# Kernel optimization log

Hardware: AMD Instinct MI355X
Metric: run time of the kernel (lower is better)

Reference implementation:

```python
import jax, jax.numpy as jnp
import numpy as np

KV_POOL = 2


def setup_inputs() -> dict:
    key = jax.random.key(0)
    ks = jax.random.split(key, 12)
    B, C1, C2, H, W, D = 8, 256, 512, 64, 64, 64
    s = 0.02
    return {
        "x1": jax.random.normal(ks[0], (B, C1, H, W), jnp.float32),
        "x2": jax.random.normal(ks[1], (B, C2, H, W), jnp.float32),
        "Wq": jax.random.normal(ks[2], (D, C1), jnp.float32) * s,
        "bq": jnp.zeros((D,), jnp.float32),
        "Wk": jax.random.normal(ks[3], (D, C2), jnp.float32) * s,
        "bk": jnp.zeros((D,), jnp.float32),
        "Wv": jax.random.normal(ks[4], (D, C2), jnp.float32) * s,
        "bv": jnp.zeros((D,), jnp.float32),
        "Wo": jax.random.normal(ks[5], (C1, D), jnp.float32) * s,
        "bo": jnp.zeros((C1,), jnp.float32),
    }


def reference(x1, x2, Wq, bq, Wk, bk, Wv, bv, Wo, bo):
    B, C1, H, W = x1.shape
    D = Wq.shape[0]
    # adaptive_avg_pool2d to (H//2, W//2) with even dims == 2x2 mean pool
    Bs, C2, H2, W2 = x2.shape
    x2p = x2.reshape(Bs, C2, H2 // KV_POOL, KV_POOL, W2 // KV_POOL, KV_POOL).mean(axis=(3, 5))
    # 1x1 convs as channel matmuls; flatten spatial dims
    Q = jnp.einsum('bchw,dc->bhwd', x1, Wq).reshape(B, H * W, D) + bq          # [B,N,D]
    K = jnp.einsum('bchw,dc->bhwd', x2p, Wk).reshape(B, -1, D) + bk            # [B,M,D]
    V = jnp.einsum('bchw,dc->bhwd', x2p, Wv).reshape(B, -1, D) + bv            # [B,M,D]
    attn = jax.nn.softmax(jnp.einsum('bnd,bmd->bnm', Q, K), axis=-1)           # [B,N,M]
    out = jnp.einsum('bnm,bmd->bnd', attn, V)                                  # [B,N,D]
    y = jnp.einsum('bnd,cd->bnc', out, Wo) + bo                                # [B,N,C1]
    y = y.reshape(B, H, W, C1).transpose(0, 3, 1, 2)                           # [B,C1,H,W]
    return x1 + y
```

## Files before the change

### kernel.cpp

```cpp
#include <hip/hip_runtime.h>
#include <hip/hip_bf16.h>

typedef __bf16 bf16x4 __attribute__((ext_vector_type(4)));
typedef __bf16 bf16x8 __attribute__((ext_vector_type(8)));
typedef float f32x16 __attribute__((ext_vector_type(16)));
typedef unsigned int u32x4 __attribute__((ext_vector_type(4)));

static constexpr int Bc = 8, C1 = 256, C2 = 512, Hh = 64, Ww = 64, Dd = 64;
static constexpr int Nn = 4096, Mm = 1024;

#define MFMA __builtin_amdgcn_mfma_f32_32x32x16_bf16

__device__ __forceinline__ uint32_t pkbf(float a, float b) {
  union { __bf16 h[2]; uint32_t u; } x;
  x.h[0] = (__bf16)a; x.h[1] = (__bf16)b;
  return x.u;
}

__device__ __forceinline__ void pack16(const float* p, bf16x8& f0, bf16x8& f1) {
  uint32_t w01 = pkbf(p[0], p[1]),   w23 = pkbf(p[2], p[3]);
  uint32_t w45 = pkbf(p[4], p[5]),   w67 = pkbf(p[6], p[7]);
  uint32_t w89 = pkbf(p[8], p[9]),   wab = pkbf(p[10], p[11]);
  uint32_t wcd = pkbf(p[12], p[13]), wef = pkbf(p[14], p[15]);
  auto s0 = __builtin_amdgcn_permlane32_swap(w01, w45, false, false);
  auto s1 = __builtin_amdgcn_permlane32_swap(w23, w67, false, false);
  auto s2 = __builtin_amdgcn_permlane32_swap(w89, wcd, false, false);
  auto s3 = __builtin_amdgcn_permlane32_swap(wab, wef, false, false);
  u32x4 q0 = {s0[0], s1[0], s0[1], s1[1]};
  u32x4 q1 = {s2[0], s3[0], s2[1], s3[1]};
  f0 = __builtin_bit_cast(bf16x8, q0);
  f1 = __builtin_bit_cast(bf16x8, q1);
}


__global__ __launch_bounds__(256) void k_prep_w(
    const float* __restrict__ Wq, const float* __restrict__ Wk,
    const float* __restrict__ Wv, const float* __restrict__ Wo,
    __bf16* __restrict__ wqb, __bf16* __restrict__ wkb,
    __bf16* __restrict__ wvb, __bf16* __restrict__ wob) {
  int i = blockIdx.x * 256 + threadIdx.x;
  if (i < 16384) wqb[i] = (__bf16)Wq[i];
  else if (i < 49152) wkb[i - 16384] = (__bf16)Wk[i - 16384];
  else if (i < 81920) wvb[i - 49152] = (__bf16)Wv[i - 49152];
  else if (i < 98304) wob[i - 81920] = (__bf16)Wo[i - 81920];
}

__global__ __launch_bounds__(256) void k_qproj(
    const float* __restrict__ x1, const __bf16* __restrict__ wqb,
    const float* __restrict__ bq, __bf16* __restrict__ qfb) {
  __shared__ __align__(16) __bf16 lds[64 * 264];
  const int b = blockIdx.y, n0 = blockIdx.x * 64, tid = threadIdx.x;
#pragma unroll 4
  for (int it = 0; it < 64; ++it) {
    int c = it * 4 + (tid >> 6);
    int j = tid & 63;
    lds[j * 264 + c] = (__bf16)x1[(size_t)(b * C1 + c) * Nn + n0 + j];
  }
  __syncthreads();
  const int w = tid >> 6, l = tid & 63, h = l >> 5, nl = l & 31;
  const int nsub = w & 1, dh = w >> 1;
  const __bf16* arow = lds + (nsub * 32 + nl) * 264;
  const __bf16* wrow = wqb + (dh * 32 + nl) * C1 + 8 * h;
  f32x16 acc = {};
#pragma unroll
  for (int ks = 0; ks < 16; ++ks) {
    bf16x8 a = *(const bf16x8*)(arow + ks * 16 + 8 * h);
    bf16x8 bb = *(const bf16x8*)(wrow + ks * 16);
    acc = MFMA(a, bb, acc, 0, 0, 0);
  }
  const int d = dh * 32 + nl;
  const float bias = bq[d];
  __bf16* qdst = qfb + (size_t)b * Nn * Dd + (size_t)((n0 >> 5) + nsub) * 2048 +
                 (d >> 4) * 512 + ((d >> 3) & 1) * 256 + (d & 7);
#pragma unroll
  for (int r = 0; r < 16; ++r) {
    int mrow = (r & 3) + 8 * (r >> 2) + 4 * h;
    qdst[mrow * 8] = (__bf16)(acc[r] + bias);
  }
}

__global__ __launch_bounds__(256) void k_kvproj(
    const float* __restrict__ x2, const __bf16* __restrict__ wkb,
    const __bf16* __restrict__ wvb, const float* __restrict__ bk,
    const float* __restrict__ bv, __bf16* __restrict__ kfb,
    __bf16* __restrict__ vfb) {
  __shared__ __align__(16) __bf16 lds[32 * 520];
  __shared__ __align__(16) __bf16 vlds[64 * 40];
  const int b = blockIdx.y, h2 = blockIdx.x, tid = threadIdx.x;
#pragma unroll 4
  for (int it = 0; it < 64; ++it) {
    int c = it * 8 + (tid >> 5);
    int j = tid & 31;
    const float* p = x2 + ((size_t)(b * C2 + c) * Hh + 2 * h2) * Ww + 2 * j;
    float2 v0 = *(const float2*)p;
    float2 v1 = *(const float2*)(p + Ww);
    lds[j * 520 + c] = (__bf16)((v0.x + v0.y + v1.x + v1.y) * 0.25f);
  }
  __syncthreads();
  const int w = tid >> 6, l = tid & 63, h = l >> 5, nl = l & 31;
  const int isv = w >> 1, dh = w & 1;
  const __bf16* arow = lds + nl * 520;
  const __bf16* wrow = (isv ? wvb : wkb) + (dh * 32 + nl) * C2 + 8 * h;
  f32x16 acc = {};
#pragma unroll
  for (int ks = 0; ks < 32; ++ks) {
    bf16x8 a = *(const bf16x8*)(arow + ks * 16 + 8 * h);
    bf16x8 bb = *(const bf16x8*)(wrow + ks * 16);
    acc = MFMA(a, bb, acc, 0, 0, 0);
  }
  const int d = dh * 32 + nl;
  const float bias = isv ? bv[d] : bk[d];
  if (!isv) {
    __bf16* kdst = kfb + (size_t)b * Mm * Dd + (size_t)h2 * 2048 +
                   (d >> 4) * 512 + ((d >> 3) & 1) * 256 + (d & 7);
#pragma unroll
    for (int r = 0; r < 16; ++r) {
      int mr = (r & 3) + 8 * (r >> 2) + 4 * h;
      kdst[mr * 8] = (__bf16)(acc[r] + bias);
    }
  } else {
#pragma unroll
    for (int r = 0; r < 16; ++r) {
      int mr = (r & 3) + 8 * (r >> 2) + 4 * h;
      vlds[d * 40 + mr] = (__bf16)(acc[r] + bias);
    }
  }
  __syncthreads();
  const int dd = tid >> 2, q = tid & 3;
  bf16x8 vv = *(const bf16x8*)(vlds + dd * 40 + q * 8);
  const int c = (q >> 1) * 2 + (dd >> 5);
  const int ll = (q & 1) * 32 + (dd & 31);
  *(bf16x8*)(vfb + (size_t)b * Mm * Dd + (size_t)h2 * 2048 + c * 512 + ll * 8) = vv;
}

template <int S>
__global__ __launch_bounds__(256) void k_attn_part(
    const __bf16* __restrict__ qfb, const __bf16* __restrict__ kfb,
    const __bf16* __restrict__ vfb, __bf16* __restrict__ po,
    float* __restrict__ pml) {
  __shared__ __align__(16) __bf16 kls[2][2048];
  __shared__ __align__(16) __bf16 vls[2][2048];
  const int lin = blockIdx.x;
  const int b = lin & 7, rest = lin >> 3, nblk = rest & 31, sp = rest >> 5;
  const int tid = threadIdx.x;
  const int w = tid >> 6, l = tid & 63, h = l >> 5, nl = l & 31;
  const int n = nblk * 128 + w * 32 + nl;
  constexpr int NT = Mm / S / 32;
  const int t0 = sp * NT;

  const __bf16* qt = qfb + (size_t)b * Nn * Dd + (size_t)(nblk * 4 + w) * 2048 + l * 8;
  bf16x8 qf0 = *(const bf16x8*)(qt);
  bf16x8 qf1 = *(const bf16x8*)(qt + 512);
  bf16x8 qf2 = *(const bf16x8*)(qt + 1024);
  bf16x8 qf3 = *(const bf16x8*)(qt + 1536);

  const __bf16* kgb = kfb + (size_t)b * Mm * Dd + (size_t)t0 * 2048 + w * 512 + l * 8;
  const __bf16* vgb = vfb + (size_t)b * Mm * Dd + (size_t)t0 * 2048 + w * 512 + l * 8;

  bf16x8 kcur = *(const bf16x8*)kgb;
  bf16x8 vcur = *(const bf16x8*)vgb;

  f32x16 o0 = {}, o1 = {};
  float lsum = 0.f;
  const int wofs = w * 512 + l * 8;

#pragma unroll
  for (int i = 0; i < NT; ++i) {
    const int cur = i & 1;
    *(bf16x8*)(&kls[cur][wofs]) = kcur;
    *(bf16x8*)(&vls[cur][wofs]) = vcur;
    __syncthreads();
    if (i + 1 < NT) {
      kcur = *(const bf16x8*)(kgb + (size_t)(i + 1) * 2048);
      vcur = *(const bf16x8*)(vgb + (size_t)(i + 1) * 2048);
    }
    bf16x8 ka0 = *(const bf16x8*)(&kls[cur][l * 8]);
    bf16x8 ka1 = *(const bf16x8*)(&kls[cur][512 + l * 8]);
    bf16x8 ka2 = *(const bf16x8*)(&kls[cur][1024 + l * 8]);
    bf16x8 ka3 = *(const bf16x8*)(&kls[cur][1536 + l * 8]);
    bf16x8 v00 = *(const bf16x8*)(&vls[cur][l * 8]);
    bf16x8 v10 = *(const bf16x8*)(&vls[cur][512 + l * 8]);
    bf16x8 v01 = *(const bf16x8*)(&vls[cur][1024 + l * 8]);
    bf16x8 v11 = *(const bf16x8*)(&vls[cur][1536 + l * 8]);
    f32x16 s = {};
    s = MFMA(ka0, qf0, s, 0, 0, 0);
    s = MFMA(ka1, qf1, s, 0, 0, 0);
    s = MFMA(ka2, qf2, s, 0, 0, 0);
    s = MFMA(ka3, qf3, s, 0, 0, 0);
    float p[16];
#pragma unroll
    for (int r = 0; r < 16; ++r) p[r] = __expf(s[r]);
    float u0 = (p[0] + p[1]) + (p[2] + p[3]);
    float u1 = (p[4] + p[5]) + (p[6] + p[7]);
    float u2 = (p[8] + p[9]) + (p[10] + p[11]);
    float u3 = (p[12] + p[13]) + (p[14] + p[15]);
    lsum += (u0 + u1) + (u2 + u3);
    bf16x8 pb0, pb1;
    pack16(p, pb0, pb1);
    o0 = MFMA(v00, pb0, o0, 0, 0, 0);
    o1 = MFMA(v10, pb0, o1, 0, 0, 0);
    o0 = MFMA(v01, pb1, o0, 0, 0, 0);
    o1 = MFMA(v11, pb1, o1, 0, 0, 0);
    __syncthreads();
  }

  const float ltot = lsum + __shfl_xor(lsum, 32);
  __bf16* ob = po + (size_t)(b * S + sp) * 16 * Nn * 4 + (size_t)n * 4;
#pragma unroll
  for (int q = 0; q < 4; ++q) {
    bf16x4 t0v, t1v;
#pragma unroll
    for (int e = 0; e < 4; ++e) {
      t0v[e] = (__bf16)o0[q * 4 + e];
      t1v[e] = (__bf16)o1[q * 4 + e];
    }
    *(bf16x4*)(ob + (size_t)(2 * q + h) * Nn * 4) = t0v;
    *(bf16x4*)(ob + (size_t)(8 + 2 * q + h) * Nn * 4) = t1v;
  }
  if (h == 0) pml[(size_t)(b * S + sp) * Nn + n] = ltot;
}

template <int S>
__global__ __launch_bounds__(256) void k_attn_comb(
    const float* __restrict__ x1, const __bf16* __restrict__ po,
    const float* __restrict__ pml, const __bf16* __restrict__ wob,
    const float* __restrict__ bo, float* __restrict__ out) {
  const int lin = blockIdx.x;
  const int b = lin & 7, rest = lin >> 3, nblk = rest & 31, ctg = rest >> 5;
  const int tid = threadIdx.x;
  const int w = tid >> 6, l = tid & 63, h = l >> 5, nl = l & 31;
  const int n = nblk * 128 + w * 32 + nl;

  float L = 0.f;
#pragma unroll
  for (int s = 0; s < S; ++s)
    L += pml[(size_t)(b * S + s) * Nn + n];
  const float inv = 1.f / L;

  float o[32];
#pragma unroll
  for (int r = 0; r < 32; ++r) o[r] = 0.f;
#pragma unroll
  for (int s = 0; s < S; ++s) {
    const __bf16* ob = po + (size_t)(b * S + s) * 16 * Nn * 4 + (size_t)n * 4;
#pragma unroll
    for (int q = 0; q < 4; ++q) {
      bf16x4 v0 = *(const bf16x4*)(ob + (size_t)(2 * q + h) * Nn * 4);
      bf16x4 v1 = *(const bf16x4*)(ob + (size_t)(8 + 2 * q + h) * Nn * 4);
#pragma unroll
      for (int e = 0; e < 4; ++e) {
        o[q * 4 + e] += (float)v0[e];
        o[16 + q * 4 + e] += (float)v1[e];
      }
    }
  }

  bf16x8 obf[4];
#pragma unroll
  for (int a2 = 0; a2 < 2; ++a2) {
    float ov[16];
#pragma unroll
    for (int r = 0; r < 16; ++r) ov[r] = o[a2 * 16 + r] * inv;
    pack16(ov, obf[a2 * 2], obf[a2 * 2 + 1]);
  }

  const float* x1r = x1 + (size_t)b * C1 * Nn + n;
  float* outr = out + (size_t)b * C1 * Nn + n;
  const __bf16* wobase = wob + (size_t)nl * Dd + 8 * h;
#pragma unroll
  for (int ci = 0; ci < 4; ++ci) {
    const int ct = ctg * 4 + ci;
    f32x16 y = {};
    const __bf16* wr = wobase + (size_t)ct * 32 * Dd;
#pragma unroll
    for (int ks = 0; ks < 4; ++ks) {
      bf16x8 a = *(const bf16x8*)(wr + ks * 16);
      y = MFMA(a, obf[ks], y, 0, 0, 0);
    }
#pragma unroll
    for (int r = 0; r < 16; ++r) {
      int c = ct * 32 + (r & 3) + 8 * (r >> 2) + 4 * h;
      size_t idx = (size_t)c * Nn;
      outr[idx] = y[r] + bo[c] + x1r[idx];
    }
  }
}

__global__ __launch_bounds__(256) void k_attn(
    const float* __restrict__ x1, const __bf16* __restrict__ qfb,
    const __bf16* __restrict__ kfb, const __bf16* __restrict__ vfb,
    const __bf16* __restrict__ wob, const float* __restrict__ bo,
    float* __restrict__ out) {
  const int b = blockIdx.y, tid = threadIdx.x;
  const int w = tid >> 6, l = tid & 63, h = l >> 5, nl = l & 31;
  const int n = blockIdx.x * 128 + w * 32 + nl;

  const __bf16* qt = qfb + (size_t)b * Nn * Dd + (size_t)(blockIdx.x * 4 + w) * 2048 + l * 8;
  bf16x8 qf0 = *(const bf16x8*)(qt);
  bf16x8 qf1 = *(const bf16x8*)(qt + 512);
  bf16x8 qf2 = *(const bf16x8*)(qt + 1024);
  bf16x8 qf3 = *(const bf16x8*)(qt + 1536);

  f32x16 o0 = {}, o1 = {};
  float mrun = -INFINITY, lsum = 0.f;

  const __bf16* kb_ = kfb + (size_t)b * Mm * Dd + l * 8;
  const __bf16* vb_ = vfb + (size_t)b * Mm * Dd + l * 8;

  for (int t = 0; t < 32; ++t) {
    const __bf16* kt = kb_ + (size_t)t * 2048;
    const __bf16* vt = vb_ + (size_t)t * 2048;
    bf16x8 ka0 = *(const bf16x8*)(kt);
    bf16x8 ka1 = *(const bf16x8*)(kt + 512);
    bf16x8 ka2 = *(const bf16x8*)(kt + 1024);
    bf16x8 ka3 = *(const bf16x8*)(kt + 1536);
    bf16x8 v00 = *(const bf16x8*)(vt);
    bf16x8 v10 = *(const bf16x8*)(vt + 512);
    bf16x8 v01 = *(const bf16x8*)(vt + 1024);
    bf16x8 v11 = *(const bf16x8*)(vt + 1536);
    f32x16 s = {};
    s = MFMA(ka0, qf0, s, 0, 0, 0);
    s = MFMA(ka1, qf1, s, 0, 0, 0);
    s = MFMA(ka2, qf2, s, 0, 0, 0);
    s = MFMA(ka3, qf3, s, 0, 0, 0);
    float tmax = s[0];
#pragma unroll
    for (int r = 1; r < 16; ++r) tmax = fmaxf(tmax, s[r]);
    tmax = fmaxf(tmax, __shfl_xor(tmax, 32));
    const float mnew = fmaxf(mrun, tmax);
    const float scale = __expf(mrun - mnew);
    float p[16], psum = 0.f;
#pragma unroll
    for (int r = 0; r < 16; ++r) { p[r] = __expf(s[r] - mnew); psum += p[r]; }
    lsum = lsum * scale + psum;
    mrun = mnew;
#pragma unroll
    for (int r = 0; r < 16; ++r) { o0[r] *= scale; o1[r] *= scale; }
    bf16x8 pb0, pb1;
    pack16(p, pb0, pb1);
    o0 = MFMA(v00, pb0, o0, 0, 0, 0);
    o1 = MFMA(v10, pb0, o1, 0, 0, 0);
    o0 = MFMA(v01, pb1, o0, 0, 0, 0);
    o1 = MFMA(v11, pb1, o1, 0, 0, 0);
  }

  const float ltot = lsum + __shfl_xor(lsum, 32);
  const float inv = 1.f / ltot;

  bf16x8 ob[4];
#pragma unroll
  for (int a2 = 0; a2 < 2; ++a2) {
    float ov[16];
#pragma unroll
    for (int r = 0; r < 16; ++r) ov[r] = (a2 ? o1[r] : o0[r]) * inv;
    pack16(ov, ob[a2 * 2], ob[a2 * 2 + 1]);
  }

  const float* x1r = x1 + (size_t)b * C1 * Nn + n;
  float* outr = out + (size_t)b * C1 * Nn + n;
  const __bf16* wobase = wob + (size_t)nl * Dd + 8 * h;
#pragma unroll 2
  for (int ct = 0; ct < 8; ++ct) {
    f32x16 y = {};
    const __bf16* wr = wobase + (size_t)ct * 32 * Dd;
#pragma unroll
    for (int ks = 0; ks < 4; ++ks) {
      bf16x8 a = *(const bf16x8*)(wr + ks * 16);
      y = MFMA(a, ob[ks], y, 0, 0, 0);
    }
#pragma unroll
    for (int r = 0; r < 16; ++r) {
      int c = ct * 32 + (r & 3) + 8 * (r >> 2) + 4 * h;
      size_t idx = (size_t)c * Nn;
      outr[idx] = y[r] + bo[c] + x1r[idx];
    }
  }
}

extern "C" void kernel_launch(void* const* d_in, const int* in_sizes, int n_in,
                              void* d_out, int out_size, void* d_ws,
                              size_t ws_size, hipStream_t stream) {
  const float* x1 = (const float*)d_in[0];
  const float* x2 = (const float*)d_in[1];
  const float* Wq = (const float*)d_in[2];
  const float* bq = (const float*)d_in[3];
  const float* Wk = (const float*)d_in[4];
  const float* bk = (const float*)d_in[5];
  const float* Wv = (const float*)d_in[6];
  const float* bv = (const float*)d_in[7];
  const float* Wo = (const float*)d_in[8];
  const float* bo = (const float*)d_in[9];
  float* out = (float*)d_out;
  char* ws = (char*)d_ws;

  __bf16* wqb = (__bf16*)(ws);
  __bf16* wkb = (__bf16*)(ws + 32768);
  __bf16* wvb = (__bf16*)(ws + 98304);
  __bf16* wob = (__bf16*)(ws + 163840);
  __bf16* qfb = (__bf16*)(ws + 196608);
  __bf16* kfb = (__bf16*)(ws + 4390912);
  __bf16* vfb = (__bf16*)(ws + 5439488);
  __bf16* po  = (__bf16*)(ws + 6488064);
  const size_t ws8 = 6488064ull + 33554432ull + 1048576ull;
  const size_t ws4 = 6488064ull + 16777216ull + 524288ull;

  hipLaunchKernelGGL(k_prep_w, dim3(384), dim3(256), 0, stream,
                     Wq, Wk, Wv, Wo, wqb, wkb, wvb, wob);
  hipLaunchKernelGGL(k_qproj, dim3(64, 8), dim3(256), 0, stream,
                     x1, wqb, bq, qfb);
  hipLaunchKernelGGL(k_kvproj, dim3(32, 8), dim3(256), 0, stream,
                     x2, wkb, wvb, bk, bv, kfb, vfb);
  if (ws_size >= ws8) {
    float* pml = (float*)(ws + 6488064 + 33554432);
    hipLaunchKernelGGL(k_attn_part<8>, dim3(32 * 8 * 8), dim3(256), 0, stream,
                       qfb, kfb, vfb, po, pml);
    hipLaunchKernelGGL(k_attn_comb<8>, dim3(32 * 8 * 2), dim3(256), 0, stream,
                       x1, po, pml, wob, bo, out);
  } else if (ws_size >= ws4) {
    float* pml = (float*)(ws + 6488064 + 16777216);
    hipLaunchKernelGGL(k_attn_part<4>, dim3(32 * 8 * 4), dim3(256), 0, stream,
                       qfb, kfb, vfb, po, pml);
    hipLaunchKernelGGL(k_attn_comb<4>, dim3(32 * 8 * 2), dim3(256), 0, stream,
                       x1, po, pml, wob, bo, out);
  } else {
    hipLaunchKernelGGL(k_attn, dim3(32, 8), dim3(256), 0, stream,
                       x1, qfb, kfb, vfb, wob, bo, out);
  }
}
```

Baseline: 67.63 us.

## Fuse projections into one kernel, convert weights inline, drop LDS staging in attention

Removes the separate weight-conversion kernel by converting fp32 weights to bf16 on the fly at load time. Merges the Q and K/V projection kernels into a single launch that splits work by block index. In the partial attention kernel, each wave now loads the full K/V tile directly from global memory into registers with prefetching, replacing the shared-memory staging and its two barriers per step. This cuts launch count and synchronisation, but every wave now re-reads K/V from global memory or cache and weight conversion is repeated per block.

```diff
diff --git a/kernel.cpp b/kernel.cpp
--- a/kernel.cpp
+++ b/kernel.cpp
@@ -15,6 +15,15 @@
   union { __bf16 h[2]; uint32_t u; } x;
   x.h[0] = (__bf16)a; x.h[1] = (__bf16)b;
   return x.u;
+}
+
+__device__ __forceinline__ bf16x8 cvt8(const float* __restrict__ p) {
+  float4 a = *(const float4*)p;
+  float4 b2 = *(const float4*)(p + 4);
+  bf16x8 r;
+  r[0] = (__bf16)a.x; r[1] = (__bf16)a.y; r[2] = (__bf16)a.z; r[3] = (__bf16)a.w;
+  r[4] = (__bf16)b2.x; r[5] = (__bf16)b2.y; r[6] = (__bf16)b2.z; r[7] = (__bf16)b2.w;
+  return r;
 }
 
 __device__ __forceinline__ void pack16(const float* p, bf16x8& f0, bf16x8& f1) {
@@ -33,104 +42,93 @@
 }
 
 
-__global__ __launch_bounds__(256) void k_prep_w(
-    const float* __restrict__ Wq, const float* __restrict__ Wk,
-    const float* __restrict__ Wv, const float* __restrict__ Wo,
-    __bf16* __restrict__ wqb, __bf16* __restrict__ wkb,
-    __bf16* __restrict__ wvb, __bf16* __restrict__ wob) {
-  int i = blockIdx.x * 256 + threadIdx.x;
-  if (i < 16384) wqb[i] = (__bf16)Wq[i];
-  else if (i < 49152) wkb[i - 16384] = (__bf16)Wk[i - 16384];
-  else if (i < 81920) wvb[i - 49152] = (__bf16)Wv[i - 49152];
-  else if (i < 98304) wob[i - 81920] = (__bf16)Wo[i - 81920];
-}
-
-__global__ __launch_bounds__(256) void k_qproj(
-    const float* __restrict__ x1, const __bf16* __restrict__ wqb,
-    const float* __restrict__ bq, __bf16* __restrict__ qfb) {
-  __shared__ __align__(16) __bf16 lds[64 * 264];
-  const int b = blockIdx.y, n0 = blockIdx.x * 64, tid = threadIdx.x;
+__global__ __launch_bounds__(256) void k_proj(
+    const float* __restrict__ x1, const float* __restrict__ x2,
+    const float* __restrict__ Wq, const float* __restrict__ bq,
+    const float* __restrict__ Wk, const float* __restrict__ bk,
+    const float* __restrict__ Wv, const float* __restrict__ bv,
+    __bf16* __restrict__ qfb, __bf16* __restrict__ kfb,
+    __bf16* __restrict__ vfb) {
+  __shared__ __align__(16) __bf16 lds[32 * 520 + 64 * 40];
+  const int bx = blockIdx.x, b = blockIdx.y, tid = threadIdx.x;
+  const int w = tid >> 6, l = tid & 63, h = l >> 5, nl = l & 31;
+
+  if (bx < 64) {
+    const int n0 = bx * 64;
 #pragma unroll 4
-  for (int it = 0; it < 64; ++it) {
-    int c = it * 4 + (tid >> 6);
-    int j = tid & 63;
-    lds[j * 264 + c] = (__bf16)x1[(size_t)(b * C1 + c) * Nn + n0 + j];
-  }
-  __syncthreads();
-  const int w = tid >> 6, l = tid & 63, h = l >> 5, nl = l & 31;
-  const int nsub = w & 1, dh = w >> 1;
-  const __bf16* arow = lds + (nsub * 32 + nl) * 264;
-  const __bf16* wrow = wqb + (dh * 32 + nl) * C1 + 8 * h;
-  f32x16 acc = {};
-#pragma unroll
-  for (int ks = 0; ks < 16; ++ks) {
-    bf16x8 a = *(const bf16x8*)(arow + ks * 16 + 8 * h);
-    bf16x8 bb = *(const bf16x8*)(wrow + ks * 16);
-    acc = MFMA(a, bb, acc, 0, 0, 0);
-  }
-  const int d = dh * 32 + nl;
-  const float bias = bq[d];
-  __bf16* qdst = qfb + (size_t)b * Nn * Dd + (size_t)((n0 >> 5) + nsub) * 2048 +
-                 (d >> 4) * 512 + ((d >> 3) & 1) * 256 + (d & 7);
-#pragma unroll
-  for (int r = 0; r < 16; ++r) {
-    int mrow = (r & 3) + 8 * (r >> 2) + 4 * h;
-    qdst[mrow * 8] = (__bf16)(acc[r] + bias);
-  }
-}
-
-__global__ __launch_bounds__(256) void k_kvproj(
-    const float* __restrict__ x2, const __bf16* __restrict__ wkb,
-    const __bf16* __restrict__ wvb, const float* __restrict__ bk,
-    const float* __restrict__ bv, __bf16* __restrict__ kfb,
-    __bf16* __restrict__ vfb) {
-  __shared__ __align__(16) __bf16 lds[32 * 520];
-  __shared__ __align__(16) __bf16 vlds[64 * 40];
-  const int b = blockIdx.y, h2 = blockIdx.x, tid = threadIdx.x;
+    for (int it = 0; it < 64; ++it) {
+      int c = it * 4 + (tid >> 6);
+      int j = tid & 63;
+      lds[j * 264 + c] = (__bf16)x1[(size_t)(b * C1 + c) * Nn + n0 + j];
+    }
+    __syncthreads();
+    const int nsub = w & 1, dh = w >> 1;
+    const __bf16* arow = lds + (nsub * 32 + nl) * 264;
+    const float* wrow = Wq + (size_t)(dh * 32 + nl) * C1 + 8 * h;
+    f32x16 acc = {};
+#pragma unroll
+    for (int ks = 0; ks < 16; ++ks) {
+      bf16x8 a = *(const bf16x8*)(arow + ks * 16 + 8 * h);
+      bf16x8 bb = cvt8(wrow + ks * 16);
+      acc = MFMA(a, bb, acc, 0, 0, 0);
+    }
+    const int d = dh * 32 + nl;
+    const float bias = bq[d];
+    __bf16* qdst = qfb + (size_t)b * Nn * Dd + (size_t)((n0 >> 5) + nsub) * 2048 +
+                   (d >> 4) * 512 + ((d >> 3) & 1) * 256 + (d & 7);
+#pragma unroll
+    for (int r = 0; r < 16; ++r) {
+      int mrow = (r & 3) + 8 * (r >> 2) + 4 * h;
+      qdst[mrow * 8] = (__bf16)(acc[r] + bias);
+    }
+  } else {
+    const int h2 = bx - 64;
+    __bf16* klds = lds;
+    __bf16* vlds = lds + 32 * 520;
 #pragma unroll 4
-  for (int it = 0; it < 64; ++it) {
-    int c = it * 8 + (tid >> 5);
-    int j = tid & 31;
-    const float* p = x2 + ((size_t)(b * C2 + c) * Hh + 2 * h2) * Ww + 2 * j;
-    float2 v0 = *(const float2*)p;
-    float2 v1 = *(const float2*)(p + Ww);
-    lds[j * 520 + c] = (__bf16)((v0.x + v0.y + v1.x + v1.y) * 0.25f);
-  }
-  __syncthreads();
-  const int w = tid >> 6, l = tid & 63, h = l >> 5, nl = l & 31;
-  const int isv = w >> 1, dh = w & 1;
-  const __bf16* arow = lds + nl * 520;
-  const __bf16* wrow = (isv ? wvb : wkb) + (dh * 32 + nl) * C2 + 8 * h;
-  f32x16 acc = {};
-#pragma unroll
-  for (int ks = 0; ks < 32; ++ks) {
-    bf16x8 a = *(const bf16x8*)(arow + ks * 16 + 8 * h);
-    bf16x8 bb = *(const bf16x8*)(wrow + ks * 16);
-    acc = MFMA(a, bb, acc, 0, 0, 0);
-  }
-  const int d = dh * 32 + nl;
-  const float bias = isv ? bv[d] : bk[d];
-  if (!isv) {
-    __bf16* kdst = kfb + (size_t)b * Mm * Dd + (size_t)h2 * 2048 +
-                   (d >> 4) * 512 + ((d >> 3) & 1) * 256 + (d & 7);
-#pragma unroll
-    for (int r = 0; r < 16; ++r) {
-      int mr = (r & 3) + 8 * (r >> 2) + 4 * h;
-      kdst[mr * 8] = (__bf16)(acc[r] + bias);
-    }
-  } else {
-#pragma unroll
-    for (int r = 0; r < 16; ++r) {
-      int mr = (r & 3) + 8 * (r >> 2) + 4 * h;
-      vlds[d * 40 + mr] = (__bf16)(acc[r] + bias);
-    }
-  }
-  __syncthreads();
-  const int dd = tid >> 2, q = tid & 3;
-  bf16x8 vv = *(const bf16x8*)(vlds + dd * 40 + q * 8);
-  const int c = (q >> 1) * 2 + (dd >> 5);
-  const int ll = (q & 1) * 32 + (dd & 31);
-  *(bf16x8*)(vfb + (size_t)b * Mm * Dd + (size_t)h2 * 2048 + c * 512 + ll * 8) = vv;
+    for (int it = 0; it < 64; ++it) {
+      int c = it * 8 + (tid >> 5);
+      int j = tid & 31;
+      const float* p = x2 + ((size_t)(b * C2 + c) * Hh + 2 * h2) * Ww + 2 * j;
+      float2 v0 = *(const float2*)p;
+      float2 v1 = *(const float2*)(p + Ww);
+      klds[j * 520 + c] = (__bf16)((v0.x + v0.y + v1.x + v1.y) * 0.25f);
+    }
+    __syncthreads();
+    const int isv = w >> 1, dh = w & 1;
+    const __bf16* arow = klds + nl * 520;
+    const float* wrow = (isv ? Wv : Wk) + (size_t)(dh * 32 + nl) * C2 + 8 * h;
+    f32x16 acc = {};
+#pragma unroll
+    for (int ks = 0; ks < 32; ++ks) {
+      bf16x8 a = *(const bf16x8*)(arow + ks * 16 + 8 * h);
+      bf16x8 bb = cvt8(wrow + ks * 16);
+      acc = MFMA(a, bb, acc, 0, 0, 0);
+    }
+    const int d = dh * 32 + nl;
+    const float bias = isv ? bv[d] : bk[d];
+    if (!isv) {
+      __bf16* kdst = kfb + (size_t)b * Mm * Dd + (size_t)h2 * 2048 +
+                     (d >> 4) * 512 + ((d >> 3) & 1) * 256 + (d & 7);
+#pragma unroll
+      for (int r = 0; r < 16; ++r) {
+        int mr = (r & 3) + 8 * (r >> 2) + 4 * h;
+        kdst[mr * 8] = (__bf16)(acc[r] + bias);
+      }
+    } else {
+#pragma unroll
+      for (int r = 0; r < 16; ++r) {
+        int mr = (r & 3) + 8 * (r >> 2) + 4 * h;
+        vlds[d * 40 + mr] = (__bf16)(acc[r] + bias);
+      }
+    }
+    __syncthreads();
+    const int dd = tid >> 2, q = tid & 3;
+    bf16x8 vv = *(const bf16x8*)(vlds + dd * 40 + q * 8);
+    const int c = (q >> 1) * 2 + (dd >> 5);
+    const int ll = (q & 1) * 32 + (dd & 31);
+    *(bf16x8*)(vfb + (size_t)b * Mm * Dd + (size_t)h2 * 2048 + c * 512 + ll * 8) = vv;
+  }
 }
 
 template <int S>
@@ -138,8 +136,6 @@
     const __bf16* __restrict__ qfb, const __bf16* __restrict__ kfb,
     const __bf16* __restrict__ vfb, __bf16* __restrict__ po,
     float* __restrict__ pml) {
-  __shared__ __align__(16) __bf16 kls[2][2048];
-  __shared__ __align__(16) __bf16 vls[2][2048];
   const int lin = blockIdx.x;
   const int b = lin & 7, rest = lin >> 3, nblk = rest & 31, sp = rest >> 5;
   const int tid = threadIdx.x;
@@ -154,39 +150,41 @@
   bf16x8 qf2 = *(const bf16x8*)(qt + 1024);
   bf16x8 qf3 = *(const bf16x8*)(qt + 1536);
 
-  const __bf16* kgb = kfb + (size_t)b * Mm * Dd + (size_t)t0 * 2048 + w * 512 + l * 8;
-  const __bf16* vgb = vfb + (size_t)b * Mm * Dd + (size_t)t0 * 2048 + w * 512 + l * 8;
-
-  bf16x8 kcur = *(const bf16x8*)kgb;
-  bf16x8 vcur = *(const bf16x8*)vgb;
+  const __bf16* kt = kfb + (size_t)b * Mm * Dd + (size_t)t0 * 2048 + l * 8;
+  const __bf16* vt = vfb + (size_t)b * Mm * Dd + (size_t)t0 * 2048 + l * 8;
 
   f32x16 o0 = {}, o1 = {};
   float lsum = 0.f;
-  const int wofs = w * 512 + l * 8;
+
+  bf16x8 ck0 = *(const bf16x8*)(kt);
+  bf16x8 ck1 = *(const bf16x8*)(kt + 512);
+  bf16x8 ck2 = *(const bf16x8*)(kt + 1024);
+  bf16x8 ck3 = *(const bf16x8*)(kt + 1536);
+  bf16x8 cv0 = *(const bf16x8*)(vt);
+  bf16x8 cv1 = *(const bf16x8*)(vt + 512);
+  bf16x8 cv2 = *(const bf16x8*)(vt + 1024);
+  bf16x8 cv3 = *(const bf16x8*)(vt + 1536);
 
 #pragma unroll
   for (int i = 0; i < NT; ++i) {
-    const int cur = i & 1;
-    *(bf16x8*)(&kls[cur][wofs]) = kcur;
-    *(bf16x8*)(&vls[cur][wofs]) = vcur;
-    __syncthreads();
+    bf16x8 nk0, nk1, nk2, nk3, nv0, nv1, nv2, nv3;
     if (i + 1 < NT) {
-      kcur = *(const bf16x8*)(kgb + (size_t)(i + 1) * 2048);
-      vcur = *(const bf16x8*)(vgb + (size_t)(i + 1) * 2048);
-    }
-    bf16x8 ka0 = *(const bf16x8*)(&kls[cur][l * 8]);
-    bf16x8 ka1 = *(const bf16x8*)(&kls[cur][512 + l * 8]);
-    bf16x8 ka2 = *(const bf16x8*)(&kls[cur][1024 + l * 8]);
-    bf16x8 ka3 = *(const bf16x8*)(&kls[cur][1536 + l * 8]);
-    bf16x8 v00 = *(const bf16x8*)(&vls[cur][l * 8]);
-    bf16x8 v10 = *(const bf16x8*)(&vls[cur][512 + l * 8]);
-    bf16x8 v01 = *(const bf16x8*)(&vls[cur][1024 + l * 8]);
-    bf16x8 v11 = *(const bf16x8*)(&vls[cur][1536 + l * 8]);
+      const __bf16* kn = kt + (size_t)(i + 1) * 2048;
+      const __bf16* vn = vt + (size_t)(i + 1) * 2048;
+      nk0 = *(const bf16x8*)(kn);
+      nk1 = *(const bf16x8*)(kn + 512);
+      nk2 = *(const bf16x8*)(kn + 1024);
+      nk3 = *(const bf16x8*)(kn + 1536);
+      nv0 = *(const bf16x8*)(vn);
+      nv1 = *(const bf16x8*)(vn + 512);
+      nv2 = *(const bf16x8*)(vn + 1024);
+      nv3 = *(const bf16x8*)(vn + 1536);
+    }
     f32x16 s = {};
-    s = MFMA(ka0, qf0, s, 0, 0, 0);
-    s = MFMA(ka1, qf1, s, 0, 0, 0);
-    s = MFMA(ka2, qf2, s, 0, 0, 0);
-    s = MFMA(ka3, qf3, s, 0, 0, 0);
+    s = MFMA(ck0, qf0, s, 0, 0, 0);
+    s = MFMA(ck1, qf1, s, 0, 0, 0);
+    s = MFMA(ck2, qf2, s, 0, 0, 0);
+    s = MFMA(ck3, qf3, s, 0, 0, 0);
     float p[16];
 #pragma unroll
     for (int r = 0; r < 16; ++r) p[r] = __expf(s[r]);
@@ -197,11 +195,14 @@
     lsum += (u0 + u1) + (u2 + u3);
     bf16x8 pb0, pb1;
     pack16(p, pb0, pb1);
-    o0 = MFMA(v00, pb0, o0, 0, 0, 0);
-    o1 = MFMA(v10, pb0, o1, 0, 0, 0);
-    o0 = MFMA(v01, pb1, o0, 0, 0, 0);
-    o1 = MFMA(v11, pb1, o1, 0, 0, 0);
-    __syncthreads();
+    o0 = MFMA(cv0, pb0, o0, 0, 0, 0);
+    o1 = MFMA(cv1, pb0, o1, 0, 0, 0);
+    o0 = MFMA(cv2, pb1, o0, 0, 0, 0);
+    o1 = MFMA(cv3, pb1, o1, 0, 0, 0);
+    if (i + 1 < NT) {
+      ck0 = nk0; ck1 = nk1; ck2 = nk2; ck3 = nk3;
+      cv0 = nv0; cv1 = nv1; cv2 = nv2; cv3 = nv3;
+    }
   }
 
   const float ltot = lsum + __shfl_xor(lsum, 32);
@@ -223,7 +224,7 @@
 template <int S>
 __global__ __launch_bounds__(256) void k_attn_comb(
     const float* __restrict__ x1, const __bf16* __restrict__ po,
-    const float* __restrict__ pml, const __bf16* __restrict__ wob,
+    const float* __restrict__ pml, const float* __restrict__ Wo,
     const float* __restrict__ bo, float* __restrict__ out) {
   const int lin = blockIdx.x;
   const int b = lin & 7, rest = lin >> 3, nblk = rest & 31, ctg = rest >> 5;
@@ -266,15 +267,15 @@
 
   const float* x1r = x1 + (size_t)b * C1 * Nn + n;
   float* outr = out + (size_t)b * C1 * Nn + n;
-  const __bf16* wobase = wob + (size_t)nl * Dd + 8 * h;
+  const float* wobase = Wo + (size_t)nl * Dd + 8 * h;
 #pragma unroll
   for (int ci = 0; ci < 4; ++ci) {
     const int ct = ctg * 4 + ci;
     f32x16 y = {};
-    const __bf16* wr = wobase + (size_t)ct * 32 * Dd;
+    const float* wr = wobase + (size_t)ct * 32 * Dd;
 #pragma unroll
     for (int ks = 0; ks < 4; ++ks) {
-      bf16x8 a = *(const bf16x8*)(wr + ks * 16);
+      bf16x8 a = cvt8(wr + ks * 16);
       y = MFMA(a, obf[ks], y, 0, 0, 0);
     }
 #pragma unroll
@@ -289,7 +290,7 @@
 __global__ __launch_bounds__(256) void k_attn(
     const float* __restrict__ x1, const __bf16* __restrict__ qfb,
     const __bf16* __restrict__ kfb, const __bf16* __restrict__ vfb,
-    const __bf16* __restrict__ wob, const float* __restrict__ bo,
+    const float* __restrict__ Wo, const float* __restrict__ bo,
     float* __restrict__ out) {
   const int b = blockIdx.y, tid = threadIdx.x;
   const int w = tid >> 6, l = tid & 63, h = l >> 5, nl = l & 31;
@@ -358,14 +359,14 @@
 
   const float* x1r = x1 + (size_t)b * C1 * Nn + n;
   float* outr = out + (size_t)b * C1 * Nn + n;
-  const __bf16* wobase = wob + (size_t)nl * Dd + 8 * h;
+  const float* wobase = Wo + (size_t)nl * Dd + 8 * h;
 #pragma unroll 2
   for (int ct = 0; ct < 8; ++ct) {
     f32x16 y = {};
-    const __bf16* wr = wobase + (size_t)ct * 32 * Dd;
+    const float* wr = wobase + (size_t)ct * 32 * Dd;
 #pragma unroll
     for (int ks = 0; ks < 4; ++ks) {
-      bf16x8 a = *(const bf16x8*)(wr + ks * 16);
+      bf16x8 a = cvt8(wr + ks * 16);
       y = MFMA(a, ob[ks], y, 0, 0, 0);
     }
 #pragma unroll
@@ -393,37 +394,29 @@
   float* out = (float*)d_out;
   char* ws = (char*)d_ws;
 
-  __bf16* wqb = (__bf16*)(ws);
-  __bf16* wkb = (__bf16*)(ws + 32768);
-  __bf16* wvb = (__bf16*)(ws + 98304);
-  __bf16* wob = (__bf16*)(ws + 163840);
-  __bf16* qfb = (__bf16*)(ws + 196608);
-  __bf16* kfb = (__bf16*)(ws + 4390912);
-  __bf16* vfb = (__bf16*)(ws + 5439488);
-  __bf16* po  = (__bf16*)(ws + 6488064);
-  const size_t ws8 = 6488064ull + 33554432ull + 1048576ull;
-  const size_t ws4 = 6488064ull + 16777216ull + 524288ull;
-
-  hipLaunchKernelGGL(k_prep_w, dim3(384), dim3(256), 0, stream,
-                     Wq, Wk, Wv, Wo, wqb, wkb, wvb, wob);
-  hipLaunchKernelGGL(k_qproj, dim3(64, 8), dim3(256), 0, stream,
-                     x1, wqb, bq, qfb);
-  hipLaunchKernelGGL(k_kvproj, dim3(32, 8), dim3(256), 0, stream,
-                     x2, wkb, wvb, bk, bv, kfb, vfb);
+  __bf16* qfb = (__bf16*)(ws);
+  __bf16* kfb = (__bf16*)(ws + 4194304);
+  __bf16* vfb = (__bf16*)(ws + 5242880);
+  __bf16* po  = (__bf16*)(ws + 6291456);
+  const size_t ws8 = 6291456ull + 33554432ull + 1048576ull;
+  const size_t ws4 = 6291456ull + 16777216ull + 524288ull;
+
+  hipLaunchKernelGGL(k_proj, dim3(96, 8), dim3(256), 0, stream,
+                     x1, x2, Wq, bq, Wk, bk, Wv, bv, qfb, kfb, vfb);
   if (ws_size >= ws8) {
-    float* pml = (float*)(ws + 6488064 + 33554432);
+    float* pml = (float*)(ws + 6291456 + 33554432);
     hipLaunchKernelGGL(k_attn_part<8>, dim3(32 * 8 * 8), dim3(256), 0, stream,
                        qfb, kfb, vfb, po, pml);
     hipLaunchKernelGGL(k_attn_comb<8>, dim3(32 * 8 * 2), dim3(256), 0, stream,
-                       x1, po, pml, wob, bo, out);
+                       x1, po, pml, Wo, bo, out);
   } else if (ws_size >= ws4) {
-    float* pml = (float*)(ws + 6488064 + 16777216);
+    float* pml = (float*)(ws + 6291456 + 16777216);
     hipLaunchKernelGGL(k_attn_part<4>, dim3(32 * 8 * 4), dim3(256), 0, stream,
                        qfb, kfb, vfb, po, pml);
     hipLaunchKernelGGL(k_attn_comb<4>, dim3(32 * 8 * 2), dim3(256), 0, stream,
-                       x1, po, pml, wob, bo, out);
+                       x1, po, pml, Wo, bo, out);
   } else {
     hipLaunchKernelGGL(k_attn, dim3(32, 8), dim3(256), 0, stream,
-                       x1, qfb, kfb, vfb, wob, bo, out);
-  }
-}
+                       x1, qfb, kfb, vfb, Wo, bo, out);
+  }
+}
```

New measurement: 72.21 us. +6.8%, slower.
